# Kernel tuning notes

Measured on AMD Instinct MI355X. Metric: run time of the kernel, lower is better.

## Reference

```python
import jax, jax.numpy as jnp
import numpy as np


def setup_inputs() -> dict:
    key = jax.random.key(0)
    k0, k1, k2, k3, k4 = jax.random.split(key, 5)
    B, W, C, C2, D = 4, 64, 512, 512, 64  # D = C // k, k=8
    x = jax.random.normal(k0, (B, W, W, C), dtype=jnp.float32)
    input_h = jax.random.normal(k1, (B, W, W, C2), dtype=jnp.float32)
    f = jax.random.normal(k2, (1, 1, C2, D), dtype=jnp.float32) * 0.02
    g = jax.random.normal(k3, (1, 1, C, D), dtype=jnp.float32) * 0.02
    gamma = jax.random.uniform(k4, (1,), dtype=jnp.float32)
    return {"x": x, "input_h": input_h, "f": f, "g": g, "gamma": gamma}


def reference(x, input_h, f, g, gamma):
    # x: [B,W,W,C] NHWC, input_h: [B,W,W,C2], f: [1,1,C2,D], g: [1,1,C,D]
    B, W, _, C = x.shape
    C2 = input_h.shape[-1]
    N = W * W
    # 1x1 convs == per-pixel channel matmuls
    f_proj = jnp.einsum('bhwc,cd->bhwd', input_h, f[0, 0])  # [B,W,W,D]
    g_proj = jnp.einsum('bhwc,cd->bhwd', x, g[0, 0])        # [B,W,W,D]
    f_flat = f_proj.reshape(B, N, -1)
    g_flat = g_proj.reshape(B, N, -1)
    # unscaled attention scores over spatial positions
    s = jnp.einsum('bnd,bmd->bnm', g_flat, f_flat)          # [B,N,N]
    beta = jax.nn.softmax(s, axis=-1)
    h_flat = input_h.reshape(B, N, C2)
    o = jnp.einsum('bnm,bmc->bnc', beta, h_flat).reshape(B, W, W, C2)
    # mix_concat == 'mix': learned residual mix
    return gamma * o + x
```

## Files before the change

kernel.cpp:

```cpp
#include <hip/hip_runtime.h>
#include <hip/hip_bf16.h>
#include <cstdint>
#include <cstddef>


#define NPOS 4096
#define CCH  512
#define DQK  64
#define LSTR 72

typedef __attribute__((ext_vector_type(8)))  short s8v;
typedef __attribute__((ext_vector_type(4)))  short s4v;
typedef __attribute__((ext_vector_type(4)))  float f4v;

__device__ __forceinline__ float bf2f(unsigned short u) {
    unsigned int x = ((unsigned int)u) << 16;
    return __builtin_bit_cast(float, x);
}
__device__ __forceinline__ unsigned short f2bf(float f) {
    unsigned int u = __builtin_bit_cast(unsigned int, f);
    u += 0x7fffu + ((u >> 16) & 1u);
    return (unsigned short)(u >> 16);
}

__device__ __forceinline__ void sync_lds() {
    asm volatile("s_waitcnt lgkmcnt(0)" ::: "memory");
    __builtin_amdgcn_s_barrier();
}

__global__ __launch_bounds__(256) void wt_kernel(
    const float* __restrict__ f, const float* __restrict__ g,
    unsigned short* __restrict__ fT, unsigned short* __restrict__ gT)
{
    int gid = blockIdx.x * 256 + threadIdx.x;
    for (int e = 0; e < 4; ++e) {
        int i = e * 16384 + gid;
        int which = i >> 15;
        int j = i & 32767;
        int d = j >> 9, k = j & 511;
        const float* s = which ? g : f;
        unsigned short* dst = which ? gT : fT;
        dst[j] = f2bf(s[k * 64 + d]);
    }
}

__global__ __launch_bounds__(256) void vt_kernel(
    const float* __restrict__ ih, unsigned short* __restrict__ Vt)
{
    __shared__ unsigned short T[64 * 65];
    const int tid = threadIdx.x;
    const int bidx = blockIdx.x;
    const int bb = bidx >> 9;
    const int rem = bidx & 511;
    const int ct = rem >> 6;
    const int nt = rem & 63;

    for (int p = 0; p < 4; ++p) {
        int idx = p * 256 + tid;
        int r = idx >> 4, gg = idx & 15;
        f4v v = *(const f4v*)(ih + ((size_t)bb * NPOS + nt * 64 + r) * CCH + ct * 64 + gg * 4);
        for (int j = 0; j < 4; ++j) T[r * 65 + gg * 4 + j] = f2bf(v[j]);
    }
    __syncthreads();
    for (int p = 0; p < 2; ++p) {
        int idx = p * 256 + tid;
        int c = idx >> 3, ng = idx & 7;
        unsigned short tmp[8];
        for (int j = 0; j < 8; ++j) tmp[j] = T[(ng * 8 + j) * 65 + c];
        *(s8v*)(Vt + ((size_t)bb * CCH + ct * 64 + c) * NPOS + nt * 64 + ng * 8) = *(const s8v*)tmp;
    }
}

__global__ __launch_bounds__(256) void proj_kernel(
    const float* __restrict__ x,  const float* __restrict__ ih,
    const unsigned short* __restrict__ gT, const unsigned short* __restrict__ fT,
    unsigned short* __restrict__ Qg, unsigned short* __restrict__ Kf)
{
    __shared__ __align__(16) short Alds[128 * LSTR];
    __shared__ __align__(16) short Wlds[64 * LSTR];
    const int tid = threadIdx.x;
    const int wave = tid >> 6, lane = tid & 63;
    const int n15 = lane & 15, quad = lane >> 4;
    const int which = blockIdx.x >> 7;
    const int rb = (blockIdx.x & 127) * 128;
    const float* src = which ? ih : x;
    const unsigned short* wT  = which ? fT : gT;
    unsigned short* dst = which ? Kf : Qg;

    f4v acc[2][4];
    for (int i = 0; i < 2; ++i)
        for (int j = 0; j < 4; ++j)
            acc[i][j] = f4v{0.f, 0.f, 0.f, 0.f};

    const int ar = tid >> 4, ag = tid & 15;
    f4v areg[8];
    s8v wreg[2];
    for (int p = 0; p < 8; ++p) {
        int idx = p * 256 + tid;
        int r = idx >> 4, gg = idx & 15;
        areg[p] = *(const f4v*)(src + (size_t)(rb + r) * CCH + gg * 4);
    }
    for (int p = 0; p < 2; ++p) {
        int idx = p * 256 + tid;
        int c = idx >> 3, gg = idx & 7;
        wreg[p] = *(const s8v*)(wT + (size_t)c * CCH + gg * 8);
    }
    (void)ar; (void)ag;

    for (int kc = 0; kc < 8; ++kc) {
        for (int p = 0; p < 8; ++p) {
            int idx = p * 256 + tid;
            int r = idx >> 4, gg = idx & 15;
            s4v tv;
            for (int j = 0; j < 4; ++j) tv[j] = (short)f2bf(areg[p][j]);
            *(s4v*)&Alds[r * LSTR + gg * 4] = tv;
        }
        for (int p = 0; p < 2; ++p) {
            int idx = p * 256 + tid;
            int c = idx >> 3, gg = idx & 7;
            *(s8v*)&Wlds[c * LSTR + gg * 8] = wreg[p];
        }
        if (kc < 7) {
            for (int p = 0; p < 8; ++p) {
                int idx = p * 256 + tid;
                int r = idx >> 4, gg = idx & 15;
                areg[p] = *(const f4v*)(src + (size_t)(rb + r) * CCH + (kc + 1) * 64 + gg * 4);
            }
            for (int p = 0; p < 2; ++p) {
                int idx = p * 256 + tid;
                int c = idx >> 3, gg = idx & 7;
                wreg[p] = *(const s8v*)(wT + (size_t)c * CCH + (kc + 1) * 64 + gg * 8);
            }
        }
        sync_lds();
        for (int kk = 0; kk < 2; ++kk) {
            s8v af0 = *(const s8v*)&Alds[(wave * 32 +      n15) * LSTR + kk * 32 + quad * 8];
            s8v af1 = *(const s8v*)&Alds[(wave * 32 + 16 + n15) * LSTR + kk * 32 + quad * 8];
            for (int ct = 0; ct < 4; ++ct) {
                s8v bf = *(const s8v*)&Wlds[(ct * 16 + n15) * LSTR + kk * 32 + quad * 8];
                acc[0][ct] = __builtin_amdgcn_mfma_f32_16x16x32_bf16(af0, bf, acc[0][ct], 0, 0, 0);
                acc[1][ct] = __builtin_amdgcn_mfma_f32_16x16x32_bf16(af1, bf, acc[1][ct], 0, 0, 0);
            }
        }
        sync_lds();
    }
    for (int rt = 0; rt < 2; ++rt)
        for (int ct = 0; ct < 4; ++ct)
            for (int r = 0; r < 4; ++r) {
                int row = wave * 32 + rt * 16 + quad * 4 + r;
                int col = ct * 16 + n15;
                dst[(size_t)(rb + row) * DQK + col] = f2bf(acc[rt][ct][r]);
            }
}

__global__ __launch_bounds__(1024) void flash_kernel(
    const unsigned short* __restrict__ Qg,
    const unsigned short* __restrict__ Kf,
    const unsigned short* __restrict__ Vt,
    const float* __restrict__ xin,
    const float* __restrict__ gptr,
    float* __restrict__ out)
{
    __shared__ __align__(16) short Klds[2 * 64 * LSTR];
    __shared__ __align__(16) short Plds[2 * 64 * LSTR];
    __shared__ float l_part[4][64];
    __shared__ float l_s[64];

    const int tid = threadIdx.x;
    const int wave = tid >> 6;
    const int lane = tid & 63;
    const int n15 = lane & 15, quad = lane >> 4;
    const int bid = blockIdx.x;
    const int xcd = bid & 7;
    const int b = xcd >> 1;
    const int qt = (xcd & 1) + ((bid >> 3) << 1);
    const int qbase = qt * 64;

    const float SOFT_M = 20.0f;

    f4v acc[4][2];
    for (int i = 0; i < 4; ++i)
        for (int j = 0; j < 2; ++j)
            acc[i][j] = f4v{0.f, 0.f, 0.f, 0.f};
    f4v lsum = f4v{0.f, 0.f, 0.f, 0.f};

    const int ti = wave >> 2;
    const int mi = wave & 3;
    s8v qf[2];
    {
        const unsigned short* qp =
            Qg + ((size_t)b * NPOS + qbase + ti * 16 + n15) * DQK + quad * 8;
        qf[0] = *(const s8v*)(qp);
        qf[1] = *(const s8v*)(qp + 32);
    }

    const int cb = wave * 32;
    const unsigned short* vp0 =
        Vt + ((size_t)b * CCH + cb + n15) * NPOS + quad * 8;
    const unsigned short* vp1 = vp0 + (size_t)16 * NPOS;

    const int kr = tid >> 3, kg = tid & 7;
    const unsigned short* kbase_p = Kf + ((size_t)b * NPOS + kr) * DQK + kg * 8;
    s8v kreg;
    if (tid < 512) {
        kreg = *(const s8v*)(kbase_p);
        *(s8v*)&Klds[kr * LSTR + kg * 8] = kreg;
        kreg = *(const s8v*)(kbase_p + (size_t)64 * DQK);
    }
    s8v vfc[2][2];
    vfc[0][0] = *(const s8v*)(vp0);
    vfc[0][1] = *(const s8v*)(vp0 + 32);
    vfc[1][0] = *(const s8v*)(vp1);
    vfc[1][1] = *(const s8v*)(vp1 + 32);
    sync_lds();

    for (int kb = 0; kb < NPOS / 64; ++kb) {
        const int m0 = kb * 64;
        const int mn = (kb + 1 < NPOS / 64) ? m0 + 64 : m0;
        s8v vfn[2][2];
        vfn[0][0] = *(const s8v*)(vp0 + mn);
        vfn[0][1] = *(const s8v*)(vp0 + mn + 32);
        vfn[1][0] = *(const s8v*)(vp1 + mn);
        vfn[1][1] = *(const s8v*)(vp1 + mn + 32);
        if (tid < 512 && kb + 1 < NPOS / 64) {
            *(s8v*)&Klds[((kb + 1) & 1) * 64 * LSTR + kr * LSTR + kg * 8] = kreg;
            if (kb + 2 < NPOS / 64)
                kreg = *(const s8v*)(kbase_p + (size_t)(m0 + 128) * DQK);
        }

        {
            const short* Kb = &Klds[(kb & 1) * 64 * LSTR];
            short* Pb = &Plds[(kb & 1) * 64 * LSTR];
            f4v s4 = f4v{0.f, 0.f, 0.f, 0.f};
            s8v kf0 = *(const s8v*)&Kb[(mi * 16 + n15) * LSTR + quad * 8];
            s8v kf1 = *(const s8v*)&Kb[(mi * 16 + n15) * LSTR + 32 + quad * 8];
            s4 = __builtin_amdgcn_mfma_f32_16x16x32_bf16(qf[0], kf0, s4, 0, 0, 0);
            s4 = __builtin_amdgcn_mfma_f32_16x16x32_bf16(qf[1], kf1, s4, 0, 0, 0);
            const int col = mi * 16 + n15;
            const int row0 = ti * 16 + quad * 4;
            for (int r = 0; r < 4; ++r) {
                unsigned short pb = f2bf(__expf(fminf(s4[r], 80.0f) - SOFT_M));
                Pb[(row0 + r) * LSTR + col] = (short)pb;
                lsum[r] += bf2f(pb);
            }
        }
        sync_lds();

        {
            const short* Pb = &Plds[(kb & 1) * 64 * LSTR];
            for (int kk = 0; kk < 2; ++kk) {
                for (int q4 = 0; q4 < 4; ++q4) {
                    s8v af = *(const s8v*)&Pb[(q4 * 16 + n15) * LSTR + kk * 32 + quad * 8];
                    acc[q4][0] = __builtin_amdgcn_mfma_f32_16x16x32_bf16(
                        af, vfc[0][kk], acc[q4][0], 0, 0, 0);
                    acc[q4][1] = __builtin_amdgcn_mfma_f32_16x16x32_bf16(
                        af, vfc[1][kk], acc[q4][1], 0, 0, 0);
                }
            }
        }
        vfc[0][0] = vfn[0][0]; vfc[0][1] = vfn[0][1];
        vfc[1][0] = vfn[1][0]; vfc[1][1] = vfn[1][1];
    }

    for (int d = 1; d < 16; d <<= 1)
        for (int r = 0; r < 4; ++r)
            lsum[r] += __shfl_xor(lsum[r], d);
    if (n15 == 0)
        for (int r = 0; r < 4; ++r)
            l_part[mi][ti * 16 + quad * 4 + r] = lsum[r];
    __syncthreads();
    if (tid < 64)
        l_s[tid] = l_part[0][tid] + l_part[1][tid] + l_part[2][tid] + l_part[3][tid];
    __syncthreads();

    const float gamma = gptr[0];
    for (int q4 = 0; q4 < 4; ++q4) {
        for (int r = 0; r < 4; ++r) {
            const int row = q4 * 16 + quad * 4 + r;
            const float sc = gamma / l_s[row];
            const size_t base = ((size_t)b * NPOS + qbase + row) * CCH;
            const int col0 = cb + n15;
            const int col1 = cb + 16 + n15;
            out[base + col0] = acc[q4][0][r] * sc + xin[base + col0];
            out[base + col1] = acc[q4][1][r] * sc + xin[base + col1];
        }
    }
}

extern "C" void kernel_launch(void* const* d_in, const int* in_sizes, int n_in,
                              void* d_out, int out_size, void* d_ws, size_t ws_size,
                              hipStream_t stream)
{
    const float* x     = (const float*)d_in[0];
    const float* ih    = (const float*)d_in[1];
    const float* f     = (const float*)d_in[2];
    const float* g     = (const float*)d_in[3];
    const float* gamma = (const float*)d_in[4];
    float* out = (float*)d_out;

    char* ws = (char*)d_ws;
    unsigned short* fT = (unsigned short*)(ws + 0);
    unsigned short* gT = (unsigned short*)(ws + 65536);
    unsigned short* Qg = (unsigned short*)(ws + 131072);
    unsigned short* Kf = (unsigned short*)(ws + 2228224);
    unsigned short* Vt = (unsigned short*)(ws + 4325376);

    wt_kernel<<<64, 256, 0, stream>>>(f, g, fT, gT);
    vt_kernel<<<2048, 256, 0, stream>>>(ih, Vt);
    proj_kernel<<<256, 256, 0, stream>>>(x, ih, gT, fT, Qg, Kf);
    flash_kernel<<<256, 1024, 0, stream>>>(Qg, Kf, Vt, x, gamma, out);
}
```

Before: 247.0 us.

## Warp-specialize flash kernel into score producer and PV consumer waves

Splits the 16 waves into 8 producer waves, which compute QK scores and exponentials one tile ahead into double-buffered LDS, and 8 consumer waves, each doing the PV MFMAs over 64 channels (a 4x4 accumulator tile) with raised priority. The goal is to overlap softmax/exp work with matrix multiplies and to raise MFMA density per wave. The trade-offs are more accumulator registers per consumer wave, V loads no longer prefetched a tile ahead, and half the waves sitting idle during each phase.

```diff
diff --git a/kernel.cpp b/kernel.cpp
--- a/kernel.cpp
+++ b/kernel.cpp
@@ -92,7 +92,6 @@
         for (int j = 0; j < 4; ++j)
             acc[i][j] = f4v{0.f, 0.f, 0.f, 0.f};
 
-    const int ar = tid >> 4, ag = tid & 15;
     f4v areg[8];
     s8v wreg[2];
     for (int p = 0; p < 8; ++p) {
@@ -105,7 +104,6 @@
         int c = idx >> 3, gg = idx & 7;
         wreg[p] = *(const s8v*)(wT + (size_t)c * CCH + gg * 8);
     }
-    (void)ar; (void)ag;
 
     for (int kc = 0; kc < 8; ++kc) {
         for (int p = 0; p < 8; ++p) {
@@ -163,7 +161,7 @@
 {
     __shared__ __align__(16) short Klds[2 * 64 * LSTR];
     __shared__ __align__(16) short Plds[2 * 64 * LSTR];
-    __shared__ float l_part[4][64];
+    __shared__ float l_part[2][64];
     __shared__ float l_s[64];
 
     const int tid = threadIdx.x;
@@ -177,60 +175,44 @@
     const int qbase = qt * 64;
 
     const float SOFT_M = 20.0f;
-
-    f4v acc[4][2];
-    for (int i = 0; i < 4; ++i)
-        for (int j = 0; j < 2; ++j)
-            acc[i][j] = f4v{0.f, 0.f, 0.f, 0.f};
+    const bool isA = (wave < 8);
+    const int NT = NPOS / 64;
+
+    const int ti = wave >> 1;
+    const int mi0 = (wave & 1) * 2;
+    s8v qf[2];
     f4v lsum = f4v{0.f, 0.f, 0.f, 0.f};
-
-    const int ti = wave >> 2;
-    const int mi = wave & 3;
-    s8v qf[2];
-    {
+    const int kr = tid >> 3, kg = tid & 7;
+    const unsigned short* kbase_p = Kf + ((size_t)b * NPOS + kr) * DQK + kg * 8;
+    s8v kreg;
+
+    const int cb = (wave - 8) * 64;
+    f4v acc[4][4];
+    const unsigned short* vp[4];
+
+    if (isA) {
         const unsigned short* qp =
             Qg + ((size_t)b * NPOS + qbase + ti * 16 + n15) * DQK + quad * 8;
         qf[0] = *(const s8v*)(qp);
         qf[1] = *(const s8v*)(qp + 32);
-    }
-
-    const int cb = wave * 32;
-    const unsigned short* vp0 =
-        Vt + ((size_t)b * CCH + cb + n15) * NPOS + quad * 8;
-    const unsigned short* vp1 = vp0 + (size_t)16 * NPOS;
-
-    const int kr = tid >> 3, kg = tid & 7;
-    const unsigned short* kbase_p = Kf + ((size_t)b * NPOS + kr) * DQK + kg * 8;
-    s8v kreg;
-    if (tid < 512) {
         kreg = *(const s8v*)(kbase_p);
         *(s8v*)&Klds[kr * LSTR + kg * 8] = kreg;
         kreg = *(const s8v*)(kbase_p + (size_t)64 * DQK);
-    }
-    s8v vfc[2][2];
-    vfc[0][0] = *(const s8v*)(vp0);
-    vfc[0][1] = *(const s8v*)(vp0 + 32);
-    vfc[1][0] = *(const s8v*)(vp1);
-    vfc[1][1] = *(const s8v*)(vp1 + 32);
+    } else {
+        for (int i = 0; i < 4; ++i)
+            for (int j = 0; j < 4; ++j)
+                acc[i][j] = f4v{0.f, 0.f, 0.f, 0.f};
+        const unsigned short* Vb = Vt + (size_t)b * CCH * NPOS;
+        for (int ct = 0; ct < 4; ++ct)
+            vp[ct] = Vb + (size_t)(cb + ct * 16 + n15) * NPOS + quad * 8;
+    }
     sync_lds();
 
-    for (int kb = 0; kb < NPOS / 64; ++kb) {
-        const int m0 = kb * 64;
-        const int mn = (kb + 1 < NPOS / 64) ? m0 + 64 : m0;
-        s8v vfn[2][2];
-        vfn[0][0] = *(const s8v*)(vp0 + mn);
-        vfn[0][1] = *(const s8v*)(vp0 + mn + 32);
-        vfn[1][0] = *(const s8v*)(vp1 + mn);
-        vfn[1][1] = *(const s8v*)(vp1 + mn + 32);
-        if (tid < 512 && kb + 1 < NPOS / 64) {
-            *(s8v*)&Klds[((kb + 1) & 1) * 64 * LSTR + kr * LSTR + kg * 8] = kreg;
-            if (kb + 2 < NPOS / 64)
-                kreg = *(const s8v*)(kbase_p + (size_t)(m0 + 128) * DQK);
-        }
-
-        {
-            const short* Kb = &Klds[(kb & 1) * 64 * LSTR];
-            short* Pb = &Plds[(kb & 1) * 64 * LSTR];
+    if (isA) {
+        const short* Kb = &Klds[0];
+        short* Pb = &Plds[0];
+        for (int mm = 0; mm < 2; ++mm) {
+            const int mi = mi0 + mm;
             f4v s4 = f4v{0.f, 0.f, 0.f, 0.f};
             s8v kf0 = *(const s8v*)&Kb[(mi * 16 + n15) * LSTR + quad * 8];
             s8v kf1 = *(const s8v*)&Kb[(mi * 16 + n15) * LSTR + 32 + quad * 8];
@@ -244,45 +226,83 @@
                 lsum[r] += bf2f(pb);
             }
         }
+        *(s8v*)&Klds[64 * LSTR + kr * LSTR + kg * 8] = kreg;
+        kreg = *(const s8v*)(kbase_p + (size_t)128 * DQK);
+    }
+    sync_lds();
+
+    for (int i = 0; i < NT; ++i) {
+        if (isA) {
+            if (i + 1 < NT) {
+                const short* Kb = &Klds[((i + 1) & 1) * 64 * LSTR];
+                short* Pb = &Plds[((i + 1) & 1) * 64 * LSTR];
+                for (int mm = 0; mm < 2; ++mm) {
+                    const int mi = mi0 + mm;
+                    f4v s4 = f4v{0.f, 0.f, 0.f, 0.f};
+                    s8v kf0 = *(const s8v*)&Kb[(mi * 16 + n15) * LSTR + quad * 8];
+                    s8v kf1 = *(const s8v*)&Kb[(mi * 16 + n15) * LSTR + 32 + quad * 8];
+                    s4 = __builtin_amdgcn_mfma_f32_16x16x32_bf16(qf[0], kf0, s4, 0, 0, 0);
+                    s4 = __builtin_amdgcn_mfma_f32_16x16x32_bf16(qf[1], kf1, s4, 0, 0, 0);
+                    const int col = mi * 16 + n15;
+                    const int row0 = ti * 16 + quad * 4;
+                    for (int r = 0; r < 4; ++r) {
+                        unsigned short pb = f2bf(__expf(fminf(s4[r], 80.0f) - SOFT_M));
+                        Pb[(row0 + r) * LSTR + col] = (short)pb;
+                        lsum[r] += bf2f(pb);
+                    }
+                }
+                if (i + 2 < NT)
+                    *(s8v*)&Klds[(i & 1) * 64 * LSTR + kr * LSTR + kg * 8] = kreg;
+                if (i + 3 < NT)
+                    kreg = *(const s8v*)(kbase_p + (size_t)(i + 3) * 64 * DQK);
+            }
+        } else {
+            const int m0 = i * 64;
+            s8v vf[4][2];
+            for (int ct = 0; ct < 4; ++ct) {
+                vf[ct][0] = *(const s8v*)(vp[ct] + m0);
+                vf[ct][1] = *(const s8v*)(vp[ct] + m0 + 32);
+            }
+            const short* Pb = &Plds[(i & 1) * 64 * LSTR];
+            for (int kk = 0; kk < 2; ++kk) {
+                s8v af[4];
+                for (int q4 = 0; q4 < 4; ++q4)
+                    af[q4] = *(const s8v*)&Pb[(q4 * 16 + n15) * LSTR + kk * 32 + quad * 8];
+                __builtin_amdgcn_s_setprio(1);
+                for (int q4 = 0; q4 < 4; ++q4)
+                    for (int ct = 0; ct < 4; ++ct)
+                        acc[q4][ct] = __builtin_amdgcn_mfma_f32_16x16x32_bf16(
+                            af[q4], vf[ct][kk], acc[q4][ct], 0, 0, 0);
+                __builtin_amdgcn_s_setprio(0);
+            }
+        }
         sync_lds();
-
-        {
-            const short* Pb = &Plds[(kb & 1) * 64 * LSTR];
-            for (int kk = 0; kk < 2; ++kk) {
-                for (int q4 = 0; q4 < 4; ++q4) {
-                    s8v af = *(const s8v*)&Pb[(q4 * 16 + n15) * LSTR + kk * 32 + quad * 8];
-                    acc[q4][0] = __builtin_amdgcn_mfma_f32_16x16x32_bf16(
-                        af, vfc[0][kk], acc[q4][0], 0, 0, 0);
-                    acc[q4][1] = __builtin_amdgcn_mfma_f32_16x16x32_bf16(
-                        af, vfc[1][kk], acc[q4][1], 0, 0, 0);
+    }
+
+    if (isA) {
+        for (int d = 1; d < 16; d <<= 1)
+            for (int r = 0; r < 4; ++r)
+                lsum[r] += __shfl_xor(lsum[r], d);
+        if (n15 == 0)
+            for (int r = 0; r < 4; ++r)
+                l_part[wave & 1][ti * 16 + quad * 4 + r] = lsum[r];
+    }
+    __syncthreads();
+    if (tid < 64) l_s[tid] = l_part[0][tid] + l_part[1][tid];
+    __syncthreads();
+
+    if (!isA) {
+        const float gamma = gptr[0];
+        for (int q4 = 0; q4 < 4; ++q4) {
+            for (int r = 0; r < 4; ++r) {
+                const int row = q4 * 16 + quad * 4 + r;
+                const float sc = gamma / l_s[row];
+                const size_t base = ((size_t)b * NPOS + qbase + row) * CCH;
+                for (int ct = 0; ct < 4; ++ct) {
+                    const int col = cb + ct * 16 + n15;
+                    out[base + col] = acc[q4][ct][r] * sc + xin[base + col];
                 }
             }
-        }
-        vfc[0][0] = vfn[0][0]; vfc[0][1] = vfn[0][1];
-        vfc[1][0] = vfn[1][0]; vfc[1][1] = vfn[1][1];
-    }
-
-    for (int d = 1; d < 16; d <<= 1)
-        for (int r = 0; r < 4; ++r)
-            lsum[r] += __shfl_xor(lsum[r], d);
-    if (n15 == 0)
-        for (int r = 0; r < 4; ++r)
-            l_part[mi][ti * 16 + quad * 4 + r] = lsum[r];
-    __syncthreads();
-    if (tid < 64)
-        l_s[tid] = l_part[0][tid] + l_part[1][tid] + l_part[2][tid] + l_part[3][tid];
-    __syncthreads();
-
-    const float gamma = gptr[0];
-    for (int q4 = 0; q4 < 4; ++q4) {
-        for (int r = 0; r < 4; ++r) {
-            const int row = q4 * 16 + quad * 4 + r;
-            const float sc = gamma / l_s[row];
-            const size_t base = ((size_t)b * NPOS + qbase + row) * CCH;
-            const int col0 = cb + n15;
-            const int col1 = cb + 16 + n15;
-            out[base + col0] = acc[q4][0][r] * sc + xin[base + col0];
-            out[base + col1] = acc[q4][1][r] * sc + xin[base + col1];
         }
     }
 }
```

Result: slower. 413.4 us (+67.4%).

## Software-pipeline flash loop so next tile's scores overlap current PV MFMAs

Applied to the files above, without the earlier changes.

Restructures the flash attention loop so the QK^T scores and exp for tile i+1 are computed in the same iteration as the P·V MFMAs for tile i. This cuts the loop from two barriers per tile to one, using double-buffered P and K in LDS. V fragments are now loaded at the top of each iteration instead of being prefetched one tile ahead, which may expose global load latency. It also adds a waves_per_eu hint and unroll pragmas throughout.

```diff
diff --git a/kernel.cpp b/kernel.cpp
--- a/kernel.cpp
+++ b/kernel.cpp
@@ -27,6 +27,8 @@
     asm volatile("s_waitcnt lgkmcnt(0)" ::: "memory");
     __builtin_amdgcn_s_barrier();
 }
+
+#define MFMA16(a, bfrag, c) __builtin_amdgcn_mfma_f32_16x16x32_bf16((a), (bfrag), (c), 0, 0, 0)
 
 __global__ __launch_bounds__(256) void wt_kernel(
     const float* __restrict__ f, const float* __restrict__ g,
@@ -59,6 +61,7 @@
         int idx = p * 256 + tid;
         int r = idx >> 4, gg = idx & 15;
         f4v v = *(const f4v*)(ih + ((size_t)bb * NPOS + nt * 64 + r) * CCH + ct * 64 + gg * 4);
+        #pragma unroll
         for (int j = 0; j < 4; ++j) T[r * 65 + gg * 4 + j] = f2bf(v[j]);
     }
     __syncthreads();
@@ -66,6 +69,7 @@
         int idx = p * 256 + tid;
         int c = idx >> 3, ng = idx & 7;
         unsigned short tmp[8];
+        #pragma unroll
         for (int j = 0; j < 8; ++j) tmp[j] = T[(ng * 8 + j) * 65 + c];
         *(s8v*)(Vt + ((size_t)bb * CCH + ct * 64 + c) * NPOS + nt * 64 + ng * 8) = *(const s8v*)tmp;
     }
@@ -88,44 +92,51 @@
     unsigned short* dst = which ? Kf : Qg;
 
     f4v acc[2][4];
+    #pragma unroll
     for (int i = 0; i < 2; ++i)
+        #pragma unroll
         for (int j = 0; j < 4; ++j)
             acc[i][j] = f4v{0.f, 0.f, 0.f, 0.f};
 
-    const int ar = tid >> 4, ag = tid & 15;
     f4v areg[8];
     s8v wreg[2];
+    #pragma unroll
     for (int p = 0; p < 8; ++p) {
         int idx = p * 256 + tid;
         int r = idx >> 4, gg = idx & 15;
         areg[p] = *(const f4v*)(src + (size_t)(rb + r) * CCH + gg * 4);
     }
+    #pragma unroll
     for (int p = 0; p < 2; ++p) {
         int idx = p * 256 + tid;
         int c = idx >> 3, gg = idx & 7;
         wreg[p] = *(const s8v*)(wT + (size_t)c * CCH + gg * 8);
     }
-    (void)ar; (void)ag;
 
     for (int kc = 0; kc < 8; ++kc) {
+        #pragma unroll
         for (int p = 0; p < 8; ++p) {
             int idx = p * 256 + tid;
             int r = idx >> 4, gg = idx & 15;
             s4v tv;
+            #pragma unroll
             for (int j = 0; j < 4; ++j) tv[j] = (short)f2bf(areg[p][j]);
             *(s4v*)&Alds[r * LSTR + gg * 4] = tv;
         }
+        #pragma unroll
         for (int p = 0; p < 2; ++p) {
             int idx = p * 256 + tid;
             int c = idx >> 3, gg = idx & 7;
             *(s8v*)&Wlds[c * LSTR + gg * 8] = wreg[p];
         }
         if (kc < 7) {
+            #pragma unroll
             for (int p = 0; p < 8; ++p) {
                 int idx = p * 256 + tid;
                 int r = idx >> 4, gg = idx & 15;
                 areg[p] = *(const f4v*)(src + (size_t)(rb + r) * CCH + (kc + 1) * 64 + gg * 4);
             }
+            #pragma unroll
             for (int p = 0; p < 2; ++p) {
                 int idx = p * 256 + tid;
                 int c = idx >> 3, gg = idx & 7;
@@ -133,19 +144,24 @@
             }
         }
         sync_lds();
+        #pragma unroll
         for (int kk = 0; kk < 2; ++kk) {
             s8v af0 = *(const s8v*)&Alds[(wave * 32 +      n15) * LSTR + kk * 32 + quad * 8];
             s8v af1 = *(const s8v*)&Alds[(wave * 32 + 16 + n15) * LSTR + kk * 32 + quad * 8];
+            #pragma unroll
             for (int ct = 0; ct < 4; ++ct) {
                 s8v bf = *(const s8v*)&Wlds[(ct * 16 + n15) * LSTR + kk * 32 + quad * 8];
-                acc[0][ct] = __builtin_amdgcn_mfma_f32_16x16x32_bf16(af0, bf, acc[0][ct], 0, 0, 0);
-                acc[1][ct] = __builtin_amdgcn_mfma_f32_16x16x32_bf16(af1, bf, acc[1][ct], 0, 0, 0);
+                acc[0][ct] = MFMA16(af0, bf, acc[0][ct]);
+                acc[1][ct] = MFMA16(af1, bf, acc[1][ct]);
             }
         }
         sync_lds();
     }
+    #pragma unroll
     for (int rt = 0; rt < 2; ++rt)
+        #pragma unroll
         for (int ct = 0; ct < 4; ++ct)
+            #pragma unroll
             for (int r = 0; r < 4; ++r) {
                 int row = wave * 32 + rt * 16 + quad * 4 + r;
                 int col = ct * 16 + n15;
@@ -153,7 +169,9 @@
             }
 }
 
-__global__ __launch_bounds__(1024) void flash_kernel(
+__global__ __launch_bounds__(1024)
+__attribute__((amdgpu_waves_per_eu(4, 4)))
+void flash_kernel(
     const unsigned short* __restrict__ Qg,
     const unsigned short* __restrict__ Kf,
     const unsigned short* __restrict__ Vt,
@@ -177,24 +195,28 @@
     const int qbase = qt * 64;
 
     const float SOFT_M = 20.0f;
-
-    f4v acc[4][2];
-    for (int i = 0; i < 4; ++i)
-        for (int j = 0; j < 2; ++j)
-            acc[i][j] = f4v{0.f, 0.f, 0.f, 0.f};
-    f4v lsum = f4v{0.f, 0.f, 0.f, 0.f};
+    const int NT = NPOS / 64;
+    const f4v zero4 = f4v{0.f, 0.f, 0.f, 0.f};
 
     const int ti = wave >> 2;
     const int mi = wave & 3;
-    s8v qf[2];
+    const int cb = wave * 32;
+
+    f4v acc[4][2];
+    #pragma unroll
+    for (int i = 0; i < 4; ++i) {
+        acc[i][0] = zero4;
+        acc[i][1] = zero4;
+    }
+    f4v lsum = zero4;
+
+    s8v qf0, qf1;
     {
         const unsigned short* qp =
             Qg + ((size_t)b * NPOS + qbase + ti * 16 + n15) * DQK + quad * 8;
-        qf[0] = *(const s8v*)(qp);
-        qf[1] = *(const s8v*)(qp + 32);
-    }
-
-    const int cb = wave * 32;
+        qf0 = *(const s8v*)(qp);
+        qf1 = *(const s8v*)(qp + 32);
+    }
     const unsigned short* vp0 =
         Vt + ((size_t)b * CCH + cb + n15) * NPOS + quad * 8;
     const unsigned short* vp1 = vp0 + (size_t)16 * NPOS;
@@ -202,79 +224,125 @@
     const int kr = tid >> 3, kg = tid & 7;
     const unsigned short* kbase_p = Kf + ((size_t)b * NPOS + kr) * DQK + kg * 8;
     s8v kreg;
+
     if (tid < 512) {
         kreg = *(const s8v*)(kbase_p);
         *(s8v*)&Klds[kr * LSTR + kg * 8] = kreg;
         kreg = *(const s8v*)(kbase_p + (size_t)64 * DQK);
     }
-    s8v vfc[2][2];
-    vfc[0][0] = *(const s8v*)(vp0);
-    vfc[0][1] = *(const s8v*)(vp0 + 32);
-    vfc[1][0] = *(const s8v*)(vp1);
-    vfc[1][1] = *(const s8v*)(vp1 + 32);
     sync_lds();
-
-    for (int kb = 0; kb < NPOS / 64; ++kb) {
-        const int m0 = kb * 64;
-        const int mn = (kb + 1 < NPOS / 64) ? m0 + 64 : m0;
-        s8v vfn[2][2];
-        vfn[0][0] = *(const s8v*)(vp0 + mn);
-        vfn[0][1] = *(const s8v*)(vp0 + mn + 32);
-        vfn[1][0] = *(const s8v*)(vp1 + mn);
-        vfn[1][1] = *(const s8v*)(vp1 + mn + 32);
-        if (tid < 512 && kb + 1 < NPOS / 64) {
-            *(s8v*)&Klds[((kb + 1) & 1) * 64 * LSTR + kr * LSTR + kg * 8] = kreg;
-            if (kb + 2 < NPOS / 64)
-                kreg = *(const s8v*)(kbase_p + (size_t)(m0 + 128) * DQK);
-        }
-
-        {
-            const short* Kb = &Klds[(kb & 1) * 64 * LSTR];
-            short* Pb = &Plds[(kb & 1) * 64 * LSTR];
-            f4v s4 = f4v{0.f, 0.f, 0.f, 0.f};
-            s8v kf0 = *(const s8v*)&Kb[(mi * 16 + n15) * LSTR + quad * 8];
-            s8v kf1 = *(const s8v*)&Kb[(mi * 16 + n15) * LSTR + 32 + quad * 8];
-            s4 = __builtin_amdgcn_mfma_f32_16x16x32_bf16(qf[0], kf0, s4, 0, 0, 0);
-            s4 = __builtin_amdgcn_mfma_f32_16x16x32_bf16(qf[1], kf1, s4, 0, 0, 0);
+    {
+        const short* Kb = &Klds[0];
+        short* Pb = &Plds[0];
+        s8v kf0 = *(const s8v*)&Kb[(mi * 16 + n15) * LSTR + quad * 8];
+        s8v kf1 = *(const s8v*)&Kb[(mi * 16 + n15) * LSTR + 32 + quad * 8];
+        f4v s4 = zero4;
+        s4 = MFMA16(qf0, kf0, s4);
+        s4 = MFMA16(qf1, kf1, s4);
+        const int col = mi * 16 + n15;
+        const int row0 = ti * 16 + quad * 4;
+        #pragma unroll
+        for (int r = 0; r < 4; ++r) {
+            unsigned short pb = f2bf(__expf(fminf(s4[r], 80.0f) - SOFT_M));
+            Pb[(row0 + r) * LSTR + col] = (short)pb;
+            lsum[r] += bf2f(pb);
+        }
+    }
+    if (tid < 512) {
+        *(s8v*)&Klds[64 * LSTR + kr * LSTR + kg * 8] = kreg;
+        kreg = *(const s8v*)(kbase_p + (size_t)128 * DQK);
+    }
+    sync_lds();
+
+    for (int i = 0; i < NT; ++i) {
+        const int m0 = i * 64;
+        s8v vf00 = *(const s8v*)(vp0 + m0);
+        s8v vf01 = *(const s8v*)(vp0 + m0 + 32);
+        s8v vf10 = *(const s8v*)(vp1 + m0);
+        s8v vf11 = *(const s8v*)(vp1 + m0 + 32);
+
+        const short* Pb = &Plds[(i & 1) * 64 * LSTR];
+        s8v af0_0 = *(const s8v*)&Pb[( 0 + n15) * LSTR + quad * 8];
+        s8v af1_0 = *(const s8v*)&Pb[(16 + n15) * LSTR + quad * 8];
+        s8v af2_0 = *(const s8v*)&Pb[(32 + n15) * LSTR + quad * 8];
+        s8v af3_0 = *(const s8v*)&Pb[(48 + n15) * LSTR + quad * 8];
+
+        s8v kf0, kf1;
+        const bool doA = (i + 1 < NT);
+        if (doA) {
+            const short* Kb = &Klds[((i + 1) & 1) * 64 * LSTR];
+            kf0 = *(const s8v*)&Kb[(mi * 16 + n15) * LSTR + quad * 8];
+            kf1 = *(const s8v*)&Kb[(mi * 16 + n15) * LSTR + 32 + quad * 8];
+        }
+        if (tid < 512 && i + 2 < NT) {
+            *(s8v*)&Klds[(i & 1) * 64 * LSTR + kr * LSTR + kg * 8] = kreg;
+            if (i + 3 < NT)
+                kreg = *(const s8v*)(kbase_p + (size_t)(i + 3) * 64 * DQK);
+        }
+
+        f4v s4 = zero4;
+        if (doA) {
+            s4 = MFMA16(qf0, kf0, s4);
+            s4 = MFMA16(qf1, kf1, s4);
+        }
+
+        acc[0][0] = MFMA16(af0_0, vf00, acc[0][0]);
+        acc[0][1] = MFMA16(af0_0, vf10, acc[0][1]);
+        acc[1][0] = MFMA16(af1_0, vf00, acc[1][0]);
+        acc[1][1] = MFMA16(af1_0, vf10, acc[1][1]);
+        acc[2][0] = MFMA16(af2_0, vf00, acc[2][0]);
+        acc[2][1] = MFMA16(af2_0, vf10, acc[2][1]);
+        acc[3][0] = MFMA16(af3_0, vf00, acc[3][0]);
+        acc[3][1] = MFMA16(af3_0, vf10, acc[3][1]);
+
+        s8v af0_1 = *(const s8v*)&Pb[( 0 + n15) * LSTR + 32 + quad * 8];
+        s8v af1_1 = *(const s8v*)&Pb[(16 + n15) * LSTR + 32 + quad * 8];
+        s8v af2_1 = *(const s8v*)&Pb[(32 + n15) * LSTR + 32 + quad * 8];
+        s8v af3_1 = *(const s8v*)&Pb[(48 + n15) * LSTR + 32 + quad * 8];
+
+        acc[0][0] = MFMA16(af0_1, vf01, acc[0][0]);
+        acc[0][1] = MFMA16(af0_1, vf11, acc[0][1]);
+        acc[1][0] = MFMA16(af1_1, vf01, acc[1][0]);
+        acc[1][1] = MFMA16(af1_1, vf11, acc[1][1]);
+        acc[2][0] = MFMA16(af2_1, vf01, acc[2][0]);
+        acc[2][1] = MFMA16(af2_1, vf11, acc[2][1]);
+        acc[3][0] = MFMA16(af3_1, vf01, acc[3][0]);
+        acc[3][1] = MFMA16(af3_1, vf11, acc[3][1]);
+
+        if (doA) {
+            short* Pw = &Plds[((i + 1) & 1) * 64 * LSTR];
             const int col = mi * 16 + n15;
             const int row0 = ti * 16 + quad * 4;
+            #pragma unroll
             for (int r = 0; r < 4; ++r) {
                 unsigned short pb = f2bf(__expf(fminf(s4[r], 80.0f) - SOFT_M));
-                Pb[(row0 + r) * LSTR + col] = (short)pb;
+                Pw[(row0 + r) * LSTR + col] = (short)pb;
                 lsum[r] += bf2f(pb);
             }
         }
         sync_lds();
-
-        {
-            const short* Pb = &Plds[(kb & 1) * 64 * LSTR];
-            for (int kk = 0; kk < 2; ++kk) {
-                for (int q4 = 0; q4 < 4; ++q4) {
-                    s8v af = *(const s8v*)&Pb[(q4 * 16 + n15) * LSTR + kk * 32 + quad * 8];
-                    acc[q4][0] = __builtin_amdgcn_mfma_f32_16x16x32_bf16(
-                        af, vfc[0][kk], acc[q4][0], 0, 0, 0);
-                    acc[q4][1] = __builtin_amdgcn_mfma_f32_16x16x32_bf16(
-                        af, vfc[1][kk], acc[q4][1], 0, 0, 0);
-                }
-            }
-        }
-        vfc[0][0] = vfn[0][0]; vfc[0][1] = vfn[0][1];
-        vfc[1][0] = vfn[1][0]; vfc[1][1] = vfn[1][1];
-    }
-
-    for (int d = 1; d < 16; d <<= 1)
+    }
+
+    #pragma unroll
+    for (int d = 1; d < 16; d <<= 1) {
+        #pragma unroll
         for (int r = 0; r < 4; ++r)
             lsum[r] += __shfl_xor(lsum[r], d);
-    if (n15 == 0)
+    }
+    if (n15 == 0) {
+        #pragma unroll
         for (int r = 0; r < 4; ++r)
             l_part[mi][ti * 16 + quad * 4 + r] = lsum[r];
+    }
     __syncthreads();
     if (tid < 64)
         l_s[tid] = l_part[0][tid] + l_part[1][tid] + l_part[2][tid] + l_part[3][tid];
     __syncthreads();
 
     const float gamma = gptr[0];
+    #pragma unroll
     for (int q4 = 0; q4 < 4; ++q4) {
+        #pragma unroll
         for (int r = 0; r < 4; ++r) {
             const int row = q4 * 16 + quad * 4 + r;
             const float sc = gamma / l_s[row];
```

New measurement: 266.4 us. 7.8% more time.
